# Optimization experiments

Hardware: AMD Instinct MI355X
Metric: run time of the kernel (lower is better)

Reference implementation:

```python
import jax, jax.numpy as jnp
import numpy as np

HIDDEN = 768
HEADS = 12
HEAD_DIM = HIDDEN // HEADS  # 64


def setup_inputs() -> dict:
    key = jax.random.key(0)
    k1, k2, k3 = jax.random.split(key, 3)
    B, N, C = 64, 197, HIDDEN
    hidden_states = jax.random.normal(k1, (B, N, C), dtype=jnp.float32)
    # qkv Linear: weight [C, 3C] (stored transposed for x @ W), bias [3C]
    w_qkv = jax.random.normal(k2, (C, 3 * C), dtype=jnp.float32) * (1.0 / np.sqrt(C))
    b_qkv = jax.random.normal(k3, (3 * C,), dtype=jnp.float32) * 0.02
    return {"hidden_states": hidden_states, "w_qkv": w_qkv, "b_qkv": b_qkv}


def reference(hidden_states, w_qkv, b_qkv):
    B, N, C = hidden_states.shape
    scale = HEAD_DIM ** -0.5
    qkv = hidden_states @ w_qkv + b_qkv                      # [B, N, 3C]
    qkv = qkv.reshape(B, N, 3, HEADS, HEAD_DIM)
    qkv = jnp.transpose(qkv, (2, 0, 3, 1, 4))                # [3, B, H, N, d]
    q, k, v = qkv[0], qkv[1], qkv[2]
    scores = jnp.einsum("bhqd,bhkd->bhqk", q, k) * scale     # [B, H, N, N]
    probs = jax.nn.softmax(scores, axis=-1)
    # dropout is identity in eval mode (p=0.0)
    ctx = jnp.einsum("bhqk,bhkd->bhqd", probs, v)            # [B, H, N, d]
    ctx = jnp.transpose(ctx, (0, 2, 1, 3)).reshape(B, N, C)  # [B, N, C]
    return ctx
```

## Files before the change

kernel.cpp:

```cpp
#include <hip/hip_runtime.h>

#define M_ROWS 12608
#define K_DIM  768
#define QSZ    9682944
#define XB_ELEMS 9732096

typedef __bf16 bf16x8 __attribute__((ext_vector_type(8)));
typedef float  f32x4  __attribute__((ext_vector_type(4)));

__device__ __forceinline__ unsigned short f2bf(float f) {
    unsigned u = __builtin_bit_cast(unsigned, f);
    u += 0x7fffu + ((u >> 16) & 1u);
    return (unsigned short)(u >> 16);
}

__device__ __forceinline__ void gll16(const unsigned short* g, unsigned short* l) {
    __builtin_amdgcn_global_load_lds(
        (const __attribute__((address_space(1))) unsigned int*)g,
        (__attribute__((address_space(3))) unsigned int*)l, 16, 0, 0);
}

__global__ void x2bf_kernel(const float* __restrict__ X, unsigned short* __restrict__ Xb) {
    size_t base = ((size_t)blockIdx.x * 256 + threadIdx.x) * 8;
    float4 a = *(const float4*)(X + base);
    float4 b = *(const float4*)(X + base + 4);
    ushort4 lo, hi;
    lo.x = f2bf(a.x); lo.y = f2bf(a.y); lo.z = f2bf(a.z); lo.w = f2bf(a.w);
    hi.x = f2bf(b.x); hi.y = f2bf(b.y); hi.z = f2bf(b.z); hi.w = f2bf(b.w);
    *(ushort4*)(Xb + base) = lo;
    *(ushort4*)(Xb + base + 4) = hi;
}

__global__ void wtrans_kernel(const float* __restrict__ W, unsigned short* __restrict__ Wt) {
    __shared__ float tile[32][33];
    int n0 = blockIdx.x * 32, k0 = blockIdx.y * 32;
    int tx = threadIdx.x, ty = threadIdx.y;
#pragma unroll
    for (int i = 0; i < 4; ++i)
        tile[ty + i * 8][tx] = W[(size_t)(k0 + ty + i * 8) * 2304 + n0 + tx];
    __syncthreads();
#pragma unroll
    for (int i = 0; i < 4; ++i)
        Wt[(size_t)(n0 + ty + i * 8) * K_DIM + k0 + tx] = f2bf(tile[tx][ty + i * 8]);
}

__global__ __launch_bounds__(256, 2) void qkv_gemm_kernel(
        const unsigned short* __restrict__ Xb, const unsigned short* __restrict__ Wt,
        const float* __restrict__ bias, unsigned short* __restrict__ qkv) {
    __shared__ __align__(16) unsigned short As[4096];
    __shared__ __align__(16) unsigned short Bs[4096];

    const int m0 = blockIdx.y * 128, n0 = blockIdx.x * 128;
    const int t = threadIdx.x;
    const int w = t >> 6, lane = t & 63, quad = lane >> 4, l16 = lane & 15;
    const int wr = (w >> 1) * 64, wc = (w & 1) * 64;

    const int s0 = w * 128 + lane;
    const int r0 = s0 & 127, kc0 = s0 >> 7;
    const int s1 = s0 + 64;
    const int r1 = s1 & 127, kc1 = s1 >> 7;
    const unsigned short* a0 = Xb + (size_t)(m0 + r0) * K_DIM + kc0 * 8;
    const unsigned short* a1 = Xb + (size_t)(m0 + r1) * K_DIM + kc1 * 8;
    const unsigned short* b0 = Wt + (size_t)(n0 + r0) * K_DIM + kc0 * 8;
    const unsigned short* b1 = Wt + (size_t)(n0 + r1) * K_DIM + kc1 * 8;

    f32x4 acc[4][4];
#pragma unroll
    for (int i = 0; i < 4; ++i)
#pragma unroll
        for (int j = 0; j < 4; ++j) acc[i][j] = (f32x4){0.f, 0.f, 0.f, 0.f};

    for (int k0 = 0; k0 < K_DIM; k0 += 32) {
        gll16(a0 + k0, &As[(w * 128) * 8]);
        gll16(a1 + k0, &As[(w * 128 + 64) * 8]);
        gll16(b0 + k0, &Bs[(w * 128) * 8]);
        gll16(b1 + k0, &Bs[(w * 128 + 64) * 8]);
        __syncthreads();
        bf16x8 af[4], bfr[4];
#pragma unroll
        for (int i = 0; i < 4; ++i)
            af[i] = *(const bf16x8*)&As[quad * 1024 + (wr + i * 16 + l16) * 8];
#pragma unroll
        for (int j = 0; j < 4; ++j)
            bfr[j] = *(const bf16x8*)&Bs[quad * 1024 + (wc + j * 16 + l16) * 8];
#pragma unroll
        for (int i = 0; i < 4; ++i)
#pragma unroll
            for (int j = 0; j < 4; ++j)
                acc[i][j] = __builtin_amdgcn_mfma_f32_16x16x32_bf16(af[i], bfr[j], acc[i][j], 0, 0, 0);
        __syncthreads();
    }

#pragma unroll
    for (int i = 0; i < 4; ++i) {
#pragma unroll
        for (int j = 0; j < 4; ++j) {
            int gn = n0 + wc + j * 16 + l16;
            int which = gn / 768;
            int rem = gn - which * 768;
            int hh = rem >> 6, dd = rem & 63;
            float bv = bias[gn];
#pragma unroll
            for (int r = 0; r < 4; ++r) {
                int gm = m0 + wr + i * 16 + quad * 4 + r;
                if (gm >= M_ROWS) continue;
                int bb = gm / 197;
                int tok = gm - bb * 197;
                float val = acc[i][j][r] + bv;
                if (which == 0) val *= 0.125f;
                size_t dst = (size_t)which * QSZ +
                             ((size_t)((bb * 12 + hh) * 197 + tok) * 64 + dd);
                qkv[dst] = f2bf(val);
            }
        }
    }
}

__global__ __launch_bounds__(256, 2) void attn_kernel(
        const unsigned short* __restrict__ qkv, float* __restrict__ out) {
    __shared__ __align__(16) unsigned short Ks[197 * 72];
    __shared__ __align__(16) unsigned short Vt[64 * 216];
    __shared__ __align__(16) unsigned short Ps[4 * 16 * 136];

    const int g = blockIdx.x;
    const int b = g / 12, h = g - b * 12;
    const int t = threadIdx.x, w = t >> 6, lane = t & 63;
    const int quad = lane >> 4, l16 = lane & 15;

    const size_t headoff = (size_t)(g * 197) * 64;
    const unsigned short* Qg = qkv + headoff;
    const unsigned short* Kg = qkv + (size_t)QSZ + headoff;
    const unsigned short* Vg = qkv + (size_t)2 * QSZ + headoff;

    for (int idx = t; idx < 1576; idx += 256) {
        int row = idx >> 3, c8 = (idx & 7) * 8;
        *(uint4*)&Ks[row * 72 + c8] = *(const uint4*)(Kg + (size_t)row * 64 + c8);
    }
    for (int idx = t; idx < 64 * 19; idx += 256) {
        int d = idx / 19, c = 197 + idx - d * 19;
        Vt[d * 216 + c] = 0;
    }
    for (int idx = t; idx < 1576; idx += 256) {
        int tok = idx >> 3, d0 = (idx & 7) * 8;
        ushort4 v0 = *(const ushort4*)(Vg + (size_t)tok * 64 + d0);
        ushort4 v1 = *(const ushort4*)(Vg + (size_t)tok * 64 + d0 + 4);
        Vt[(d0 + 0) * 216 + tok] = v0.x;
        Vt[(d0 + 1) * 216 + tok] = v0.y;
        Vt[(d0 + 2) * 216 + tok] = v0.z;
        Vt[(d0 + 3) * 216 + tok] = v0.w;
        Vt[(d0 + 4) * 216 + tok] = v1.x;
        Vt[(d0 + 5) * 216 + tok] = v1.y;
        Vt[(d0 + 6) * 216 + tok] = v1.z;
        Vt[(d0 + 7) * 216 + tok] = v1.w;
    }
    __syncthreads();

    unsigned short* Pw = Ps + w * (16 * 136);

    for (int tile = w; tile < 13; tile += 4) {
        int rq = tile * 16 + l16;
        int tokq = rq < 197 ? rq : 196;
        bf16x8 aq0 = *(const bf16x8*)(Qg + (size_t)tokq * 64 + quad * 8);
        bf16x8 aq1 = *(const bf16x8*)(Qg + (size_t)tokq * 64 + 32 + quad * 8);

        f32x4 s[13];
#pragma unroll
        for (int c = 0; c < 13; ++c) {
            int krow = c * 16 + l16;
            if (krow > 196) krow = 196;
            bf16x8 kb0 = *(const bf16x8*)&Ks[krow * 72 + quad * 8];
            bf16x8 kb1 = *(const bf16x8*)&Ks[krow * 72 + 32 + quad * 8];
            f32x4 zz = (f32x4){0.f, 0.f, 0.f, 0.f};
            zz = __builtin_amdgcn_mfma_f32_16x16x32_bf16(aq0, kb0, zz, 0, 0, 0);
            zz = __builtin_amdgcn_mfma_f32_16x16x32_bf16(aq1, kb1, zz, 0, 0, 0);
            s[c] = zz;
        }
        if (l16 >= 5) { s[12][0] = -1e30f; s[12][1] = -1e30f; s[12][2] = -1e30f; s[12][3] = -1e30f; }

        float mx[4], lsum[4];
#pragma unroll
        for (int r = 0; r < 4; ++r) {
            float m = s[0][r];
#pragma unroll
            for (int c = 1; c < 13; ++c) m = fmaxf(m, s[c][r]);
#pragma unroll
            for (int d = 1; d < 16; d <<= 1) m = fmaxf(m, __shfl_xor(m, d));
            mx[r] = m;
            lsum[r] = 0.f;
        }
#pragma unroll
        for (int c = 0; c < 13; ++c)
#pragma unroll
            for (int r = 0; r < 4; ++r) {
                float p = __expf(s[c][r] - mx[r]);
                s[c][r] = p;
                lsum[r] += p;
            }
#pragma unroll
        for (int r = 0; r < 4; ++r)
#pragma unroll
            for (int d = 1; d < 16; d <<= 1) lsum[r] += __shfl_xor(lsum[r], d);

        f32x4 o[4];
#pragma unroll
        for (int j = 0; j < 4; ++j) o[j] = (f32x4){0.f, 0.f, 0.f, 0.f};

#pragma unroll
        for (int c = 0; c < 8; ++c)
#pragma unroll
            for (int r = 0; r < 4; ++r)
                Pw[(quad * 4 + r) * 136 + c * 16 + l16] = f2bf(s[c][r]);
#pragma unroll
        for (int kc = 0; kc < 4; ++kc) {
            int kof = kc * 32 + quad * 8;
            bf16x8 ap = *(const bf16x8*)&Pw[l16 * 136 + kof];
#pragma unroll
            for (int j = 0; j < 4; ++j) {
                bf16x8 bv = *(const bf16x8*)&Vt[(j * 16 + l16) * 216 + kof];
                o[j] = __builtin_amdgcn_mfma_f32_16x16x32_bf16(ap, bv, o[j], 0, 0, 0);
            }
        }
#pragma unroll
        for (int r = 0; r < 4; ++r)
            Pw[(quad * 4 + r) * 136 + 80 + l16] = 0;
#pragma unroll
        for (int c = 8; c < 13; ++c)
#pragma unroll
            for (int r = 0; r < 4; ++r)
                Pw[(quad * 4 + r) * 136 + (c - 8) * 16 + l16] = f2bf(s[c][r]);
#pragma unroll
        for (int kc = 0; kc < 3; ++kc) {
            int kofA = kc * 32 + quad * 8;
            int kofB = (kc == 2 && quad >= 2) ? 0 : kofA;
            bf16x8 ap = *(const bf16x8*)&Pw[l16 * 136 + kofA];
#pragma unroll
            for (int j = 0; j < 4; ++j) {
                bf16x8 bv = *(const bf16x8*)&Vt[(j * 16 + l16) * 216 + 128 + kofB];
                o[j] = __builtin_amdgcn_mfma_f32_16x16x32_bf16(ap, bv, o[j], 0, 0, 0);
            }
        }

        int tokbase = tile * 16 + quad * 4;
#pragma unroll
        for (int r = 0; r < 4; ++r) {
            int tr = tokbase + r;
            if (tr >= 197) continue;
            float inv = 1.f / lsum[r];
#pragma unroll
            for (int j = 0; j < 4; ++j)
                out[((size_t)(b * 197 + tr)) * 768 + h * 64 + j * 16 + l16] = o[j][r] * inv;
        }
    }
}

extern "C" void kernel_launch(void* const* d_in, const int* in_sizes, int n_in,
                              void* d_out, int out_size, void* d_ws, size_t ws_size,
                              hipStream_t stream) {
    const float* X    = (const float*)d_in[0];
    const float* W    = (const float*)d_in[1];
    const float* bias = (const float*)d_in[2];
    unsigned short* ws = (unsigned short*)d_ws;
    float* out = (float*)d_out;

    unsigned short* Xb = (unsigned short*)d_out;
    unsigned short* Wt = (unsigned short*)d_out + XB_ELEMS;

    x2bf_kernel<<<4728, 256, 0, stream>>>(X, Xb);
    wtrans_kernel<<<dim3(72, 24), dim3(32, 8), 0, stream>>>(W, Wt);
    qkv_gemm_kernel<<<dim3(18, 99), 256, 0, stream>>>(Xb, Wt, bias, ws);
    attn_kernel<<<768, 256, 0, stream>>>(ws, out);
}
```

Baseline: 230.0 us.

## Rewrite QKV GEMM with 256x256 tiles, 4-stage LDS pipeline and XCD-aware block mapping

Replaces the 128x128 single-buffered QKV GEMM with 512-thread blocks computing 256x256 tiles. A 4-deep LDS ring is fed by global_load_lds prefetches three k-steps ahead and split across two barrier phases, with s_setprio around the MFMA bursts. Blocks are remapped so neighbouring tiles land on the same XCD, and X is zero-padded to 12800 rows to drop partial-tile handling. The aim is to hide global-load latency and raise data reuse per tile. The cost is higher LDS and register pressure and fewer blocks (450) to spread across CUs.

New measurement: 262.7 us. +14.2%, slower.

```diff
diff --git a/kernel.cpp b/kernel.cpp
--- a/kernel.cpp
+++ b/kernel.cpp
@@ -1,9 +1,10 @@
 #include <hip/hip_runtime.h>
 
 #define M_ROWS 12608
+#define M_PAD  12800
 #define K_DIM  768
 #define QSZ    9682944
-#define XB_ELEMS 9732096
+#define XB_ELEMS (12800*768)
 
 typedef __bf16 bf16x8 __attribute__((ext_vector_type(8)));
 typedef float  f32x4  __attribute__((ext_vector_type(4)));
@@ -20,8 +21,15 @@
         (__attribute__((address_space(3))) unsigned int*)l, 16, 0, 0);
 }
 
+__device__ __forceinline__ void cfence() { asm volatile("" ::: "memory"); }
+
 __global__ void x2bf_kernel(const float* __restrict__ X, unsigned short* __restrict__ Xb) {
     size_t base = ((size_t)blockIdx.x * 256 + threadIdx.x) * 8;
+    if (base >= (size_t)M_ROWS * K_DIM) {
+        *(ushort4*)(Xb + base) = (ushort4){0, 0, 0, 0};
+        *(ushort4*)(Xb + base + 4) = (ushort4){0, 0, 0, 0};
+        return;
+    }
     float4 a = *(const float4*)(X + base);
     float4 b = *(const float4*)(X + base + 4);
     ushort4 lo, hi;
@@ -44,68 +52,107 @@
         Wt[(size_t)(n0 + ty + i * 8) * K_DIM + k0 + tx] = f2bf(tile[tx][ty + i * 8]);
 }
 
-__global__ __launch_bounds__(256, 2) void qkv_gemm_kernel(
+__global__ __launch_bounds__(512, 2) void qkv_gemm_kernel(
         const unsigned short* __restrict__ Xb, const unsigned short* __restrict__ Wt,
         const float* __restrict__ bias, unsigned short* __restrict__ qkv) {
-    __shared__ __align__(16) unsigned short As[4096];
-    __shared__ __align__(16) unsigned short Bs[4096];
-
-    const int m0 = blockIdx.y * 128, n0 = blockIdx.x * 128;
+    __shared__ __align__(16) unsigned short As[4][8192];
+    __shared__ __align__(16) unsigned short Bs[4][8192];
+
+    const int lin = blockIdx.x;
+    const int xcd = lin & 7, ix = lin >> 3;
+    const int wg = (xcd < 2) ? xcd * 57 + ix : 114 + (xcd - 2) * 56 + ix;
+    const int by = wg / 9, bx = wg - by * 9;
+    const int m0 = by * 256, n0 = bx * 256;
+
     const int t = threadIdx.x;
     const int w = t >> 6, lane = t & 63, quad = lane >> 4, l16 = lane & 15;
-    const int wr = (w >> 1) * 64, wc = (w & 1) * 64;
-
-    const int s0 = w * 128 + lane;
-    const int r0 = s0 & 127, kc0 = s0 >> 7;
-    const int s1 = s0 + 64;
-    const int r1 = s1 & 127, kc1 = s1 >> 7;
-    const unsigned short* a0 = Xb + (size_t)(m0 + r0) * K_DIM + kc0 * 8;
-    const unsigned short* a1 = Xb + (size_t)(m0 + r1) * K_DIM + kc1 * 8;
-    const unsigned short* b0 = Wt + (size_t)(n0 + r0) * K_DIM + kc0 * 8;
-    const unsigned short* b1 = Wt + (size_t)(n0 + r1) * K_DIM + kc1 * 8;
-
-    f32x4 acc[4][4];
-#pragma unroll
-    for (int i = 0; i < 4; ++i)
+    const int wr = w >> 2, wc = w & 3;
+
+    const unsigned short* aP = Xb + (size_t)(m0 + (t & 255)) * K_DIM + (t >> 8) * 8;
+    const unsigned short* bP = Wt + (size_t)(n0 + (t & 255)) * K_DIM + (t >> 8) * 8;
+
+    const int aOff = (quad * 256 + wr * 128 + l16) * 8;
+    const int bOff = (quad * 256 + wc * 64 + l16) * 8;
+
+    f32x4 acc[8][4];
+#pragma unroll
+    for (int i = 0; i < 8; ++i)
 #pragma unroll
         for (int j = 0; j < 4; ++j) acc[i][j] = (f32x4){0.f, 0.f, 0.f, 0.f};
 
-    for (int k0 = 0; k0 < K_DIM; k0 += 32) {
-        gll16(a0 + k0, &As[(w * 128) * 8]);
-        gll16(a1 + k0, &As[(w * 128 + 64) * 8]);
-        gll16(b0 + k0, &Bs[(w * 128) * 8]);
-        gll16(b1 + k0, &Bs[(w * 128 + 64) * 8]);
-        __syncthreads();
-        bf16x8 af[4], bfr[4];
+#pragma unroll
+    for (int kt = 0; kt < 3; ++kt) {
+        gll16(aP + kt * 32,      &As[kt][w * 512]);
+        gll16(aP + kt * 32 + 16, &As[kt][4096 + w * 512]);
+        gll16(bP + kt * 32,      &Bs[kt][w * 512]);
+        gll16(bP + kt * 32 + 16, &Bs[kt][4096 + w * 512]);
+    }
+    asm volatile("s_waitcnt vmcnt(8)" ::: "memory");
+    __builtin_amdgcn_s_barrier();
+    cfence();
+
+    for (int kt = 0; kt < 24; ++kt) {
+        const int buf = kt & 3, sb = (kt + 3) & 3;
+        const unsigned short* Ab = As[buf];
+        const unsigned short* Bb = Bs[buf];
+        const int sk = (kt + 3) * 32;
+
+        bf16x8 af[4], bfj[4];
+#pragma unroll
+        for (int i = 0; i < 4; ++i) af[i] = *(const bf16x8*)&Ab[aOff + i * 128];
+#pragma unroll
+        for (int j = 0; j < 4; ++j) bfj[j] = *(const bf16x8*)&Bb[bOff + j * 128];
+        gll16(aP + sk,      &As[sb][w * 512]);
+        gll16(aP + sk + 16, &As[sb][4096 + w * 512]);
+        cfence();
+        __builtin_amdgcn_s_barrier();
+        cfence();
+        __builtin_amdgcn_s_setprio(1);
 #pragma unroll
         for (int i = 0; i < 4; ++i)
-            af[i] = *(const bf16x8*)&As[quad * 1024 + (wr + i * 16 + l16) * 8];
-#pragma unroll
-        for (int j = 0; j < 4; ++j)
-            bfr[j] = *(const bf16x8*)&Bs[quad * 1024 + (wc + j * 16 + l16) * 8];
+#pragma unroll
+            for (int j = 0; j < 4; ++j)
+                acc[i][j] = __builtin_amdgcn_mfma_f32_16x16x32_bf16(af[i], bfj[j], acc[i][j], 0, 0, 0);
+        __builtin_amdgcn_s_setprio(0);
+        cfence();
+        __builtin_amdgcn_s_barrier();
+        cfence();
+
+#pragma unroll
+        for (int i = 0; i < 4; ++i) af[i] = *(const bf16x8*)&Ab[aOff + 512 + i * 128];
+        gll16(bP + sk,      &Bs[sb][w * 512]);
+        gll16(bP + sk + 16, &Bs[sb][4096 + w * 512]);
+        cfence();
+        __builtin_amdgcn_s_barrier();
+        cfence();
+        __builtin_amdgcn_s_setprio(1);
 #pragma unroll
         for (int i = 0; i < 4; ++i)
 #pragma unroll
             for (int j = 0; j < 4; ++j)
-                acc[i][j] = __builtin_amdgcn_mfma_f32_16x16x32_bf16(af[i], bfr[j], acc[i][j], 0, 0, 0);
-        __syncthreads();
-    }
-
-#pragma unroll
-    for (int i = 0; i < 4; ++i) {
-#pragma unroll
-        for (int j = 0; j < 4; ++j) {
-            int gn = n0 + wc + j * 16 + l16;
-            int which = gn / 768;
-            int rem = gn - which * 768;
-            int hh = rem >> 6, dd = rem & 63;
-            float bv = bias[gn];
+                acc[i + 4][j] = __builtin_amdgcn_mfma_f32_16x16x32_bf16(af[i], bfj[j], acc[i + 4][j], 0, 0, 0);
+        __builtin_amdgcn_s_setprio(0);
+        asm volatile("s_waitcnt vmcnt(8)" ::: "memory");
+        __builtin_amdgcn_s_barrier();
+        cfence();
+    }
+
+    const int which = bx / 3;
+#pragma unroll
+    for (int j = 0; j < 4; ++j) {
+        const int gn = n0 + wc * 64 + j * 16 + l16;
+        const float bv = bias[gn];
+        const int rem = gn - which * 768;
+        const int hh = rem >> 6, dd = rem & 63;
+#pragma unroll
+        for (int i = 0; i < 8; ++i) {
+            const int gm0 = m0 + wr * 128 + i * 16 + quad * 4;
 #pragma unroll
             for (int r = 0; r < 4; ++r) {
-                int gm = m0 + wr + i * 16 + quad * 4 + r;
+                const int gm = gm0 + r;
                 if (gm >= M_ROWS) continue;
-                int bb = gm / 197;
-                int tok = gm - bb * 197;
+                const int bb = gm / 197;
+                const int tok = gm - bb * 197;
                 float val = acc[i][j][r] + bv;
                 if (which == 0) val *= 0.125f;
                 size_t dst = (size_t)which * QSZ +
@@ -265,8 +312,8 @@
     unsigned short* Xb = (unsigned short*)d_out;
     unsigned short* Wt = (unsigned short*)d_out + XB_ELEMS;
 
-    x2bf_kernel<<<4728, 256, 0, stream>>>(X, Xb);
+    x2bf_kernel<<<4800, 256, 0, stream>>>(X, Xb);
     wtrans_kernel<<<dim3(72, 24), dim3(32, 8), 0, stream>>>(W, Wt);
-    qkv_gemm_kernel<<<dim3(18, 99), 256, 0, stream>>>(Xb, Wt, bias, ws);
+    qkv_gemm_kernel<<<450, 512, 0, stream>>>(Xb, Wt, bias, ws);
     attn_kernel<<<768, 256, 0, stream>>>(ws, out);
 }
```

## Triple-buffer QKV GEMM LDS loads and remap blocks per XCD

Applied to the files above, without the earlier changes.

The QKV GEMM now keeps three LDS stages and prefetches two K-tiles ahead with async global-to-LDS loads. Each iteration waits on vmcnt and issues a single barrier, replacing the two __syncthreads per K step. It raises wave priority around the MFMA block and remaps the 1D grid so consecutive tiles land on the same XCD, to improve L2 reuse. The cost is triple the LDS use (48KB per block), which may limit occupancy. The last iterations issue dummy reloads of tile 0.

New measurement: 244.6 us. 1.06x slower.

```diff
diff --git a/kernel.cpp b/kernel.cpp
--- a/kernel.cpp
+++ b/kernel.cpp
@@ -47,10 +47,15 @@
 __global__ __launch_bounds__(256, 2) void qkv_gemm_kernel(
         const unsigned short* __restrict__ Xb, const unsigned short* __restrict__ Wt,
         const float* __restrict__ bias, unsigned short* __restrict__ qkv) {
-    __shared__ __align__(16) unsigned short As[4096];
-    __shared__ __align__(16) unsigned short Bs[4096];
-
-    const int m0 = blockIdx.y * 128, n0 = blockIdx.x * 128;
+    __shared__ __align__(16) unsigned short As[3][4096];
+    __shared__ __align__(16) unsigned short Bs[3][4096];
+
+    const int lin = blockIdx.x;
+    const int xcd = lin & 7, ix = lin >> 3;
+    const int wg = (xcd < 6) ? xcd * 223 + ix : 1338 + (xcd - 6) * 222 + ix;
+    const int by = wg / 18, bx = wg - by * 18;
+    const int m0 = by * 128, n0 = bx * 128;
+
     const int t = threadIdx.x;
     const int w = t >> 6, lane = t & 63, quad = lane >> 4, l16 = lane & 15;
     const int wr = (w >> 1) * 64, wc = (w & 1) * 64;
@@ -70,25 +75,47 @@
 #pragma unroll
         for (int j = 0; j < 4; ++j) acc[i][j] = (f32x4){0.f, 0.f, 0.f, 0.f};
 
-    for (int k0 = 0; k0 < K_DIM; k0 += 32) {
-        gll16(a0 + k0, &As[(w * 128) * 8]);
-        gll16(a1 + k0, &As[(w * 128 + 64) * 8]);
-        gll16(b0 + k0, &Bs[(w * 128) * 8]);
-        gll16(b1 + k0, &Bs[(w * 128 + 64) * 8]);
-        __syncthreads();
+#pragma unroll
+    for (int p = 0; p < 2; ++p) {
+        gll16(a0 + p * 32, &As[p][w * 1024]);
+        gll16(a1 + p * 32, &As[p][w * 1024 + 512]);
+        gll16(b0 + p * 32, &Bs[p][w * 1024]);
+        gll16(b1 + p * 32, &Bs[p][w * 1024 + 512]);
+    }
+    asm volatile("s_waitcnt vmcnt(4)" ::: "memory");
+    __builtin_amdgcn_s_barrier();
+    asm volatile("" ::: "memory");
+
+#pragma unroll 3
+    for (int kt = 0; kt < 24; ++kt) {
+        const int cur = kt % 3;
+        const int stb = (kt + 2) % 3;
+        const int sk = (kt + 2 < 24 ? kt + 2 : 0) * 32;
+
+        gll16(a0 + sk, &As[stb][w * 1024]);
+        gll16(a1 + sk, &As[stb][w * 1024 + 512]);
+        gll16(b0 + sk, &Bs[stb][w * 1024]);
+        gll16(b1 + sk, &Bs[stb][w * 1024 + 512]);
+
         bf16x8 af[4], bfr[4];
 #pragma unroll
         for (int i = 0; i < 4; ++i)
-            af[i] = *(const bf16x8*)&As[quad * 1024 + (wr + i * 16 + l16) * 8];
+            af[i] = *(const bf16x8*)&As[cur][quad * 1024 + (wr + i * 16 + l16) * 8];
 #pragma unroll
         for (int j = 0; j < 4; ++j)
-            bfr[j] = *(const bf16x8*)&Bs[quad * 1024 + (wc + j * 16 + l16) * 8];
+            bfr[j] = *(const bf16x8*)&Bs[cur][quad * 1024 + (wc + j * 16 + l16) * 8];
+
+        __builtin_amdgcn_s_setprio(1);
 #pragma unroll
         for (int i = 0; i < 4; ++i)
 #pragma unroll
             for (int j = 0; j < 4; ++j)
                 acc[i][j] = __builtin_amdgcn_mfma_f32_16x16x32_bf16(af[i], bfr[j], acc[i][j], 0, 0, 0);
-        __syncthreads();
+        __builtin_amdgcn_s_setprio(0);
+
+        asm volatile("s_waitcnt vmcnt(4)" ::: "memory");
+        __builtin_amdgcn_s_barrier();
+        asm volatile("" ::: "memory");
     }
 
 #pragma unroll
@@ -267,6 +294,6 @@
 
     x2bf_kernel<<<4728, 256, 0, stream>>>(X, Xb);
     wtrans_kernel<<<dim3(72, 24), dim3(32, 8), 0, stream>>>(W, Wt);
-    qkv_gemm_kernel<<<dim3(18, 99), 256, 0, stream>>>(Xb, Wt, bias, ws);
+    qkv_gemm_kernel<<<1782, 256, 0, stream>>>(Xb, Wt, bias, ws);
     attn_kernel<<<768, 256, 0, stream>>>(ws, out);
 }
```
